# Kernel optimization log

Measured on AMD Instinct MI355X. Metric: run time of the kernel, lower is better.

## Reference

```python
import jax, jax.numpy as jnp
import numpy as np

N_ITER = 5
B = 16            # graphs
NPG = 3125        # nodes per graph
EPG = 50000       # edges per graph
N_NODES = B * NPG # 50000
E = B * EPG       # 800000
F = 32            # f_e = f_x = f_u
H = 64            # hidden


def _lin(key, fan_in, fan_out):
    k1, k2 = jax.random.split(key)
    s = 1.0 / np.sqrt(fan_in)
    W = jax.random.uniform(k1, (fan_in, fan_out), jnp.float32, -s, s)
    b = jax.random.uniform(k2, (fan_out,), jnp.float32, -s, s)
    return W, b


def setup_inputs() -> dict:
    key = jax.random.key(0)
    ks = jax.random.split(key, 12)
    x = jax.random.normal(ks[0], (N_NODES, F), jnp.float32)
    edge_attr = jax.random.normal(ks[1], (E, F), jnp.float32)
    y = jax.random.normal(ks[2], (B, F), jnp.float32)
    # within-graph random edges: graph g owns nodes [g*NPG, (g+1)*NPG)
    off = (jnp.arange(B, dtype=jnp.int32) * NPG)[:, None]          # [B,1]
    src = jax.random.randint(ks[3], (B, EPG), 0, NPG, jnp.int32) + off
    dst = jax.random.randint(ks[4], (B, EPG), 0, NPG, jnp.int32) + off
    edge_index = jnp.stack([src.reshape(-1), dst.reshape(-1)])      # [2,E]
    batch = jnp.repeat(jnp.arange(B, dtype=jnp.int32), NPG)         # [N]
    # shared GN-block parameters (one block reused for all N_ITER steps)
    We1, be1 = _lin(ks[5], F + 2 * F + F, H)   # edge MLP: [src,dst,e,u[b]]
    We2, be2 = _lin(ks[6], H, F)
    Wn1, bn1 = _lin(ks[7], F + F + F, H)       # node MLP: [x,e_agg,u[b]]
    Wn2, bn2 = _lin(ks[8], H, F)
    Wg1, bg1 = _lin(ks[9], F + F + F, H)       # global MLP: [x_agg,e_agg,u]
    Wg2, bg2 = _lin(ks[10], H, F)
    return dict(x=x, edge_attr=edge_attr, y=y,
                We1=We1, be1=be1, We2=We2, be2=be2,
                Wn1=Wn1, bn1=bn1, Wn2=Wn2, bn2=bn2,
                Wg1=Wg1, bg1=bg1, Wg2=Wg2, bg2=bg2,
                edge_index=edge_index, batch=batch)


def _mlp(h_in, W1, b1, W2, b2):
    return jax.nn.relu(h_in @ W1 + b1) @ W2 + b2


def _segment_mean(vals, seg, num):
    s = jax.ops.segment_sum(vals, seg, num_segments=num)
    c = jax.ops.segment_sum(jnp.ones((vals.shape[0], 1), vals.dtype), seg,
                            num_segments=num)
    return s / jnp.maximum(c, 1.0)


def _gn_forward(x, edge_attr, y, params, edge_index, batch):
    (We1, be1, We2, be2, Wn1, bn1, Wn2, bn2, Wg1, bg1, Wg2, bg2) = params
    row, col = edge_index[0], edge_index[1]
    e_batch = batch[row]
    for _ in range(N_ITER):  # shared-weight unrolled GN block
        # EdgeModel: phi_e([src, dest, e, u[batch_e]])
        e_in = jnp.concatenate([x[row], x[col], edge_attr, y[e_batch]], axis=1)
        edge_attr = _mlp(e_in, We1, be1, We2, be2)
        # NodeModel: mean of incoming edges (scatter over col)
        e_agg_node = _segment_mean(edge_attr, col, N_NODES)
        n_in = jnp.concatenate([x, e_agg_node, y[batch]], axis=1)
        x = _mlp(n_in, Wn1, bn1, Wn2, bn2)
        # GlobalModel: per-graph means of edges and nodes
        e_agg = _segment_mean(edge_attr, e_batch, B)
        x_agg = _segment_mean(x, batch, B)
        g_in = jnp.concatenate([x_agg, e_agg, y], axis=1)
        y = _mlp(g_in, Wg1, bg1, Wg2, bg2)
    return x, edge_attr, y


def reference(x, edge_attr, y,
              We1, be1, We2, be2,
              Wn1, bn1, Wn2, bn2,
              Wg1, bg1, Wg2, bg2,
              edge_index, batch):
    params = (We1, be1, We2, be2, Wn1, bn1, Wn2, bn2, Wg1, bg1, Wg2, bg2)
    return _gn_forward(x, edge_attr, y, params, edge_index, batch)
```

## Files before the change

### kernel.cpp

```cpp
#include <hip/hip_runtime.h>

#define NITER   5
#define B_G     16
#define NPG     3125
#define EPG     50000
#define NNODES  50000
#define NEDGES  800000
#define FD      32
#define HD      64

#define EDGE_TPG   391
#define EDGE_BLOCKS 1024

#define NODE_TPG   25
#define NODE_BLOCKS (B_G * NODE_TPG)

typedef __attribute__((ext_vector_type(4))) float f32x4;
typedef __attribute__((ext_vector_type(8))) short bf16x8;
typedef __attribute__((ext_vector_type(4))) unsigned int u32x4;

union FragU { bf16x8 v; unsigned int u[4]; u32x4 q; };

__device__ __forceinline__ void fsplit2(float a, float b,
                                        unsigned int& hi, unsigned int& lo) {
    unsigned int ua = __float_as_uint(a), ub = __float_as_uint(b);
    float la = a - __uint_as_float(ua & 0xffff0000u);
    float lb = b - __uint_as_float(ub & 0xffff0000u);
    hi = __builtin_amdgcn_perm(ub, ua, 0x07060302u);
    lo = __builtin_amdgcn_perm(__float_as_uint(lb), __float_as_uint(la), 0x07060302u);
}
__device__ __forceinline__ unsigned int fpack_hl(float v) {
    unsigned int uv = __float_as_uint(v);
    float lv = v - __uint_as_float(uv & 0xffff0000u);
    return __builtin_amdgcn_perm(__float_as_uint(lv), uv, 0x07060302u);
}
__device__ __forceinline__ bf16x8 ldfrag(const unsigned int* p) {
    FragU t; t.q = *(const u32x4*)p; return t.v;
}

__global__ __launch_bounds__(1024) void wsplit_kernel(
    const float* __restrict__ We1, const float* __restrict__ We2,
    const float* __restrict__ Wn1, const float* __restrict__ Wn2,
    unsigned int* __restrict__ wsp)
{
    for (int item = threadIdx.x; item < 1792; item += 1024) {
        const float* W; unsigned int* dst; int lda, s, n, l;
        if (item < 768)       { int f = item >> 6;          l = item & 63; s = f >> 2; n = f & 3; W = We1; lda = 64; dst = wsp + f * 512; }
        else if (item < 1024) { int f = (item - 768) >> 6;  l = item & 63; s = f >> 1; n = f & 1; W = We2; lda = 32; dst = wsp + 6144 + f * 512; }
        else if (item < 1536) { int f = (item - 1024) >> 6; l = item & 63; s = f >> 2; n = f & 3; W = Wn1; lda = 64; dst = wsp + 8192 + f * 512; }
        else                  { int f = (item - 1536) >> 6; l = item & 63; s = f >> 1; n = f & 1; W = Wn2; lda = 32; dst = wsp + 12288 + f * 512; }
        int lm = l & 15, lg = l >> 4;
        int rowbase = s * 32 + lg * 8;
        int col = n * 16 + lm;
        #pragma unroll
        for (int p = 0; p < 4; ++p) {
            float a = W[(rowbase + 2 * p) * lda + col];
            float b = W[(rowbase + 2 * p + 1) * lda + col];
            unsigned int hi, lo;
            fsplit2(a, b, hi, lo);
            dst[l * 4 + p] = hi;
            dst[256 + l * 4 + p] = lo;
        }
    }
}

__global__ __launch_bounds__(256) void xsplit_kernel(
    const float* __restrict__ xin, unsigned int* __restrict__ x_sp)
{
    int t = blockIdx.x * 256 + threadIdx.x;
    if (t >= NNODES * 4) return;
    int n = t >> 2, c = t & 3;
    long base = (long)n * 32 + c * 8;
    f32x4 a = *(const f32x4*)(xin + base);
    f32x4 b = *(const f32x4*)(xin + base + 4);
    unsigned int h[4], lo[4];
    fsplit2(a[0], a[1], h[0], lo[0]);
    fsplit2(a[2], a[3], h[1], lo[1]);
    fsplit2(b[0], b[1], h[2], lo[2]);
    fsplit2(b[2], b[3], h[3], lo[3]);
    *(u32x4*)(x_sp + (long)n * 32 + c * 4)      = (u32x4){h[0], h[1], h[2], h[3]};
    *(u32x4*)(x_sp + (long)n * 32 + 16 + c * 4) = (u32x4){lo[0], lo[1], lo[2], lo[3]};
}


__global__ __launch_bounds__(256) void count_kernel(const int* __restrict__ coli,
                                                    int* __restrict__ cnt)
{
    int e = blockIdx.x * 256 + threadIdx.x;
    if (e < NEDGES) atomicAdd(&cnt[coli[e]], 1);
}

__global__ __launch_bounds__(1024) void scan_blocks_kernel(const int* __restrict__ deg,
                                                           int* __restrict__ off,
                                                           int* __restrict__ bsum, int n)
{
    __shared__ int buf[1024];
    int tid = threadIdx.x;
    int idx = blockIdx.x * 1024 + tid;
    int v = (idx < n) ? deg[idx] : 0;
    buf[tid] = v;
    __syncthreads();
    for (int o = 1; o < 1024; o <<= 1) {
        int t = (tid >= o) ? buf[tid - o] : 0;
        __syncthreads();
        buf[tid] += t;
        __syncthreads();
    }
    if (idx < n) off[idx] = buf[tid] - v;
    if (tid == 1023) bsum[blockIdx.x] = buf[1023];
}

__global__ __launch_bounds__(64) void scan_carry_kernel(int* __restrict__ bsum,
                                                        int* __restrict__ off,
                                                        int nb, int n)
{
    if (threadIdx.x == 0) {
        int c = 0;
        for (int i = 0; i < nb; ++i) { int t = bsum[i]; bsum[i] = c; c += t; }
        off[n] = c;
    }
}

__global__ __launch_bounds__(1024) void scan_add_kernel(const int* __restrict__ bsum,
                                                        int* __restrict__ off, int n)
{
    int idx = blockIdx.x * 1024 + threadIdx.x;
    if (idx < n) off[idx] += bsum[blockIdx.x];
}

__global__ __launch_bounds__(256) void fill_kernel(const int* __restrict__ coli,
                                                   const int* __restrict__ off,
                                                   int* __restrict__ cursor,
                                                   int* __restrict__ csr)
{
    int e = blockIdx.x * 256 + threadIdx.x;
    if (e < NEDGES) {
        int c = coli[e];
        int pos = atomicAdd(&cursor[c], 1);
        csr[off[c] + pos] = e;
    }
}


__global__ __launch_bounds__(1024) void prep_kernel(
    const float* __restrict__ y,
    const float* __restrict__ We1, const float* __restrict__ be1,
    const float* __restrict__ Wn1, const float* __restrict__ bn1,
    float* __restrict__ cu_e, float* __restrict__ cu_n,
    float* __restrict__ xagg, float* __restrict__ eagg)
{
    int tid = threadIdx.x;
    if (tid < B_G * FD) xagg[tid] = 0.0f;
    else                eagg[tid - B_G * FD] = 0.0f;

    int g = tid >> 6;
    int j = tid & 63;
    float ae = be1[j];
    float an = bn1[j];
    for (int k = 0; k < FD; ++k) {
        float yv = y[g * FD + k];
        ae = fmaf(yv, We1[(96 + k) * HD + j], ae);
        an = fmaf(yv, Wn1[(64 + k) * HD + j], an);
    }
    cu_e[g * HD + j] = ae;
    cu_n[g * HD + j] = an;
}

__global__ __launch_bounds__(256) void edge_mfma_kernel(
    const unsigned int* __restrict__ x_sp,
    const float* __restrict__ ea_in,
    const int* __restrict__ rowi,
    const int* __restrict__ coli,
    const unsigned int* __restrict__ wsp,
    const float* __restrict__ be2,
    const float* __restrict__ cu_e,
    float* __restrict__ ea_out,
    float* __restrict__ eagg)
{
    __shared__ unsigned int h_lds[4][32][68];

    const int tid = threadIdx.x;
    const int wid = tid >> 6;
    const int l   = tid & 63;
    const int lm  = l & 15;
    const int lg  = l >> 4;
    const int koff = lg * 8;

    bf16x8 w1h[3][4], w1l[3][4];
    #pragma unroll
    for (int s = 0; s < 3; ++s)
        #pragma unroll
        for (int n = 0; n < 4; ++n) {
            const unsigned int* p = wsp + (s * 4 + n) * 512 + l * 4;
            w1h[s][n] = ldfrag(p);
            w1l[s][n] = ldfrag(p + 256);
        }
    bf16x8 w2h[2][2], w2l[2][2];
    #pragma unroll
    for (int s = 0; s < 2; ++s)
        #pragma unroll
        for (int n = 0; n < 2; ++n) {
            const unsigned int* p = wsp + 6144 + (s * 2 + n) * 512 + l * 4;
            w2h[s][n] = ldfrag(p);
            w2l[s][n] = ldfrag(p + 256);
        }
    float bias2[2];
    bias2[0] = be2[lm];
    bias2[1] = be2[16 + lm];

    const int b   = blockIdx.x;
    const int xcd = b & 7;
    const int i   = b >> 3;
    const int g   = 2 * xcd + (i >> 6);
    const int j0  = i & 63;
    const long gbase = (long)g * EPG;
    const long gend  = gbase + EPG;

    float bcu[4];
    #pragma unroll
    for (int n = 0; n < 4; ++n) bcu[n] = cu_e[g * HD + n * 16 + lm];

    auto idx_load = [&](int (&rr)[2], int (&cc)[2], int lt) {
        #pragma unroll
        for (int t = 0; t < 2; ++t) {
            long e = gbase + (long)lt * 128 + wid * 32 + t * 16 + lm;
            if (e >= gend) e = gend - 1;
            rr[t] = rowi[e];
            cc[t] = coli[e];
        }
    };
    auto x_load = [&](u32x4 (&xh)[2][2], u32x4 (&xl)[2][2],
                      const int (&rr)[2], const int (&cc)[2]) {
        #pragma unroll
        for (int t = 0; t < 2; ++t) {
            const unsigned int* pr = x_sp + (long)rr[t] * 32;
            const unsigned int* pc = x_sp + (long)cc[t] * 32;
            xh[t][0] = *(const u32x4*)(pr + lg * 4);
            xl[t][0] = *(const u32x4*)(pr + 16 + lg * 4);
            xh[t][1] = *(const u32x4*)(pc + lg * 4);
            xl[t][1] = *(const u32x4*)(pc + 16 + lg * 4);
        }
    };

    auto compute = [&](int lt, u32x4 (&xh)[2][2], u32x4 (&xl)[2][2]) {
        const long e0 = gbase + (long)lt * 128 + wid * 32;

        f32x4 vea[2][2];
        #pragma unroll
        for (int t = 0; t < 2; ++t) {
            long e = e0 + t * 16 + lm;
            if (e >= gend) e = gend - 1;
            const float* p2 = ea_in + e * FD + koff;
            vea[t][0] = *(const f32x4*)p2;
            vea[t][1] = *(const f32x4*)(p2 + 4);
        }

        f32x4 acc1[2][4];
        #pragma unroll
        for (int n = 0; n < 4; ++n)
            #pragma unroll
            for (int t = 0; t < 2; ++t)
                acc1[t][n] = (f32x4){bcu[n], bcu[n], bcu[n], bcu[n]};

        #pragma unroll
        for (int t = 0; t < 2; ++t)
            #pragma unroll
            for (int s = 0; s < 2; ++s) {
                FragU ah, al;
                ah.q = xh[t][s];
                al.q = xl[t][s];
                #pragma unroll
                for (int n = 0; n < 4; ++n) {
                    acc1[t][n] = __builtin_amdgcn_mfma_f32_16x16x32_bf16(ah.v, w1h[s][n], acc1[t][n], 0, 0, 0);
                    acc1[t][n] = __builtin_amdgcn_mfma_f32_16x16x32_bf16(ah.v, w1l[s][n], acc1[t][n], 0, 0, 0);
                    acc1[t][n] = __builtin_amdgcn_mfma_f32_16x16x32_bf16(al.v, w1h[s][n], acc1[t][n], 0, 0, 0);
                }
            }
        #pragma unroll
        for (int t = 0; t < 2; ++t) {
            FragU ah, al;
            #pragma unroll
            for (int q = 0; q < 2; ++q)
                #pragma unroll
                for (int p = 0; p < 2; ++p)
                    fsplit2(vea[t][q][2 * p], vea[t][q][2 * p + 1],
                            ah.u[q * 2 + p], al.u[q * 2 + p]);
            #pragma unroll
            for (int n = 0; n < 4; ++n) {
                acc1[t][n] = __builtin_amdgcn_mfma_f32_16x16x32_bf16(ah.v, w1h[2][n], acc1[t][n], 0, 0, 0);
                acc1[t][n] = __builtin_amdgcn_mfma_f32_16x16x32_bf16(ah.v, w1l[2][n], acc1[t][n], 0, 0, 0);
                acc1[t][n] = __builtin_amdgcn_mfma_f32_16x16x32_bf16(al.v, w1h[2][n], acc1[t][n], 0, 0, 0);
            }
        }

        #pragma unroll
        for (int t = 0; t < 2; ++t)
            #pragma unroll
            for (int n = 0; n < 4; ++n)
                #pragma unroll
                for (int r = 0; r < 4; ++r)
                    h_lds[wid][t * 16 + lg * 4 + r][n * 16 + lm] =
                        fpack_hl(fmaxf(acc1[t][n][r], 0.0f));
        asm volatile("s_waitcnt lgkmcnt(0)" ::: "memory");
        __builtin_amdgcn_sched_barrier(0);

        f32x4 acc2[2][2];
        #pragma unroll
        for (int n = 0; n < 2; ++n)
            #pragma unroll
            for (int t = 0; t < 2; ++t)
                acc2[t][n] = (f32x4){bias2[n], bias2[n], bias2[n], bias2[n]};
        #pragma unroll
        for (int t = 0; t < 2; ++t)
            #pragma unroll
            for (int s = 0; s < 2; ++s) {
                const unsigned int* hp = &h_lds[wid][t * 16 + lm][s * 32 + koff];
                unsigned int u0 = hp[0], u1 = hp[1], u2 = hp[2], u3 = hp[3];
                unsigned int u4 = hp[4], u5 = hp[5], u6 = hp[6], u7 = hp[7];
                FragU ah, al;
                ah.u[0] = __builtin_amdgcn_perm(u1, u0, 0x05040100u);
                ah.u[1] = __builtin_amdgcn_perm(u3, u2, 0x05040100u);
                ah.u[2] = __builtin_amdgcn_perm(u5, u4, 0x05040100u);
                ah.u[3] = __builtin_amdgcn_perm(u7, u6, 0x05040100u);
                al.u[0] = __builtin_amdgcn_perm(u1, u0, 0x07060302u);
                al.u[1] = __builtin_amdgcn_perm(u3, u2, 0x07060302u);
                al.u[2] = __builtin_amdgcn_perm(u5, u4, 0x07060302u);
                al.u[3] = __builtin_amdgcn_perm(u7, u6, 0x07060302u);
                #pragma unroll
                for (int n = 0; n < 2; ++n) {
                    acc2[t][n] = __builtin_amdgcn_mfma_f32_16x16x32_bf16(ah.v, w2h[s][n], acc2[t][n], 0, 0, 0);
                    acc2[t][n] = __builtin_amdgcn_mfma_f32_16x16x32_bf16(ah.v, w2l[s][n], acc2[t][n], 0, 0, 0);
                    acc2[t][n] = __builtin_amdgcn_mfma_f32_16x16x32_bf16(al.v, w2h[s][n], acc2[t][n], 0, 0, 0);
                }
            }

        #pragma unroll
        for (int t = 0; t < 2; ++t)
            #pragma unroll
            for (int r = 0; r < 4; ++r) {
                long e = e0 + t * 16 + lg * 4 + r;
                if (e < gend) {
                    ea_out[e * FD + lm]      = acc2[t][0][r];
                    ea_out[e * FD + 16 + lm] = acc2[t][1][r];
                }
            }

        #pragma unroll
        for (int n = 0; n < 2; ++n) {
            float s = 0.0f;
            #pragma unroll
            for (int t = 0; t < 2; ++t)
                #pragma unroll
                for (int r = 0; r < 4; ++r) {
                    long e = e0 + t * 16 + lg * 4 + r;
                    s += (e < gend) ? acc2[t][n][r] : 0.0f;
                }
            s += __shfl_xor(s, 16, 64);
            s += __shfl_xor(s, 32, 64);
            if (lg == 0) atomicAdd(&eagg[g * FD + n * 16 + lm], s);
        }
    };

    int rrA[2], ccA[2], rrB[2], ccB[2];
    u32x4 xhA[2][2], xlA[2][2], xhB[2][2], xlB[2][2];

    idx_load(rrA, ccA, j0);
    x_load(xhA, xlA, rrA, ccA);
    idx_load(rrB, ccB, j0 + 64);

    auto step = [&](int lt,
                    u32x4 (&xh)[2][2], u32x4 (&xl)[2][2], int (&rrD)[2], int (&ccD)[2],
                    u32x4 (&xhN)[2][2], u32x4 (&xlN)[2][2], int (&rrN)[2], int (&ccN)[2]) {
        idx_load(rrD, ccD, lt + 128);
        x_load(xhN, xlN, rrN, ccN);
        compute(lt, xh, xl);
    };

    for (int lt = j0; lt < EDGE_TPG; lt += 128) {
        step(lt, xhA, xlA, rrA, ccA, xhB, xlB, rrB, ccB);
        if (lt + 64 < EDGE_TPG)
            step(lt + 64, xhB, xlB, rrB, ccB, xhA, xlA, rrA, ccA);
    }
}

__global__ __launch_bounds__(256) void agg_kernel(
    const float* __restrict__ ea,
    const int* __restrict__ off,
    const int* __restrict__ csr,
    float* __restrict__ e_mean)
{
    int wid = threadIdx.x >> 6;
    int l   = threadIdx.x & 63;
    int rq  = l >> 3;
    int q   = l & 7;
    int n = blockIdx.x * 4 + wid;
    int s0 = off[n], s1 = off[n + 1];
    int deg = s1 - s0;

    f32x4 acc = {0.0f, 0.0f, 0.0f, 0.0f};
    if (deg > 0) {
        int cl = (l < deg) ? l : 0;
        int cidx = csr[s0 + cl];
        #pragma unroll
        for (int r = 0; r < 8; ++r) {
            int src = r * 8 + rq;
            int eid = __shfl(cidx, src, 64);
            if (src < deg) {
                f32x4 v = *(const f32x4*)(ea + (long)eid * FD + q * 4);
                acc += v;
            }
        }
        if (deg > 64) {
            for (int i = s0 + 64; i < s1; i += 8) {
                int ii = i + rq;
                if (ii < s1) {
                    int eid = csr[ii];
                    acc += *(const f32x4*)(ea + (long)eid * FD + q * 4);
                }
            }
        }
    }
    #pragma unroll
    for (int m = 8; m < 64; m <<= 1) {
        acc[0] += __shfl_xor(acc[0], m, 64);
        acc[1] += __shfl_xor(acc[1], m, 64);
        acc[2] += __shfl_xor(acc[2], m, 64);
        acc[3] += __shfl_xor(acc[3], m, 64);
    }
    float inv = 1.0f / (float)(deg > 1 ? deg : 1);
    if (l < 8) {
        f32x4 o = {acc[0] * inv, acc[1] * inv, acc[2] * inv, acc[3] * inv};
        *(f32x4*)(e_mean + (long)n * FD + q * 4) = o;
    }
}

__global__ __launch_bounds__(256) void node_mfma_kernel(
    const float* __restrict__ x_in,
    const float* __restrict__ e_mean,
    const unsigned int* __restrict__ wsp,
    const float* __restrict__ bn2,
    const float* __restrict__ cu_n,
    float* __restrict__ x_out,
    float* __restrict__ xagg)
{
    __shared__ unsigned int h_lds[4][32][68];

    const int tid = threadIdx.x;
    const int wid = tid >> 6;
    const int l   = tid & 63;
    const int lm  = l & 15;
    const int lg  = l >> 4;
    const int koff = lg * 8;

    bf16x8 w1h[2][4], w1l[2][4];
    #pragma unroll
    for (int s = 0; s < 2; ++s)
        #pragma unroll
        for (int n = 0; n < 4; ++n) {
            const unsigned int* p = wsp + (s * 4 + n) * 512 + l * 4;
            w1h[s][n] = ldfrag(p);
            w1l[s][n] = ldfrag(p + 256);
        }
    bf16x8 w2h[2][2], w2l[2][2];
    #pragma unroll
    for (int s = 0; s < 2; ++s)
        #pragma unroll
        for (int n = 0; n < 2; ++n) {
            const unsigned int* p = wsp + 4096 + (s * 2 + n) * 512 + l * 4;
            w2h[s][n] = ldfrag(p);
            w2l[s][n] = ldfrag(p + 256);
        }
    float bias2[2];
    bias2[0] = bn2[lm];
    bias2[1] = bn2[16 + lm];

    const int g  = blockIdx.x / NODE_TPG;
    const int lt = blockIdx.x - g * NODE_TPG;
    const int nb = lt * 128 + wid * 32;

    f32x4 va[2][2][2];
    #pragma unroll
    for (int t = 0; t < 2; ++t) {
        int rl = nb + t * 16 + lm;
        if (rl > NPG - 1) rl = NPG - 1;
        long node = (long)g * NPG + rl;
        const float* p0 = x_in   + node * FD + koff;
        const float* p1 = e_mean + node * FD + koff;
        va[t][0][0] = *(const f32x4*)p0; va[t][0][1] = *(const f32x4*)(p0 + 4);
        va[t][1][0] = *(const f32x4*)p1; va[t][1][1] = *(const f32x4*)(p1 + 4);
    }

    f32x4 acc1[2][4];
    #pragma unroll
    for (int n = 0; n < 4; ++n) {
        float b = cu_n[g * HD + n * 16 + lm];
        #pragma unroll
        for (int t = 0; t < 2; ++t) acc1[t][n] = (f32x4){b, b, b, b};
    }

    #pragma unroll
    for (int t = 0; t < 2; ++t) {
        #pragma unroll
        for (int s = 0; s < 2; ++s) {
            FragU ah, al;
            #pragma unroll
            for (int q = 0; q < 2; ++q)
                #pragma unroll
                for (int p = 0; p < 2; ++p)
                    fsplit2(va[t][s][q][2 * p], va[t][s][q][2 * p + 1],
                            ah.u[q * 2 + p], al.u[q * 2 + p]);
            #pragma unroll
            for (int n = 0; n < 4; ++n) {
                acc1[t][n] = __builtin_amdgcn_mfma_f32_16x16x32_bf16(ah.v, w1h[s][n], acc1[t][n], 0, 0, 0);
                acc1[t][n] = __builtin_amdgcn_mfma_f32_16x16x32_bf16(ah.v, w1l[s][n], acc1[t][n], 0, 0, 0);
                acc1[t][n] = __builtin_amdgcn_mfma_f32_16x16x32_bf16(al.v, w1h[s][n], acc1[t][n], 0, 0, 0);
            }
        }
    }

    #pragma unroll
    for (int t = 0; t < 2; ++t)
        #pragma unroll
        for (int n = 0; n < 4; ++n)
            #pragma unroll
            for (int r = 0; r < 4; ++r)
                h_lds[wid][t * 16 + lg * 4 + r][n * 16 + lm] =
                    fpack_hl(fmaxf(acc1[t][n][r], 0.0f));
    asm volatile("s_waitcnt lgkmcnt(0)" ::: "memory");
    __builtin_amdgcn_sched_barrier(0);

    f32x4 acc2[2][2];
    #pragma unroll
    for (int n = 0; n < 2; ++n) {
        #pragma unroll
        for (int t = 0; t < 2; ++t) acc2[t][n] = (f32x4){bias2[n], bias2[n], bias2[n], bias2[n]};
    }
    #pragma unroll
    for (int t = 0; t < 2; ++t) {
        #pragma unroll
        for (int s = 0; s < 2; ++s) {
            const unsigned int* hp = &h_lds[wid][t * 16 + lm][s * 32 + koff];
            unsigned int u0 = hp[0], u1 = hp[1], u2 = hp[2], u3 = hp[3];
            unsigned int u4 = hp[4], u5 = hp[5], u6 = hp[6], u7 = hp[7];
            FragU ah, al;
            ah.u[0] = __builtin_amdgcn_perm(u1, u0, 0x05040100u);
            ah.u[1] = __builtin_amdgcn_perm(u3, u2, 0x05040100u);
            ah.u[2] = __builtin_amdgcn_perm(u5, u4, 0x05040100u);
            ah.u[3] = __builtin_amdgcn_perm(u7, u6, 0x05040100u);
            al.u[0] = __builtin_amdgcn_perm(u1, u0, 0x07060302u);
            al.u[1] = __builtin_amdgcn_perm(u3, u2, 0x07060302u);
            al.u[2] = __builtin_amdgcn_perm(u5, u4, 0x07060302u);
            al.u[3] = __builtin_amdgcn_perm(u7, u6, 0x07060302u);
            #pragma unroll
            for (int n = 0; n < 2; ++n) {
                acc2[t][n] = __builtin_amdgcn_mfma_f32_16x16x32_bf16(ah.v, w2h[s][n], acc2[t][n], 0, 0, 0);
                acc2[t][n] = __builtin_amdgcn_mfma_f32_16x16x32_bf16(ah.v, w2l[s][n], acc2[t][n], 0, 0, 0);
                acc2[t][n] = __builtin_amdgcn_mfma_f32_16x16x32_bf16(al.v, w2h[s][n], acc2[t][n], 0, 0, 0);
            }
        }
    }

    #pragma unroll
    for (int t = 0; t < 2; ++t)
        #pragma unroll
        for (int r = 0; r < 4; ++r) {
            int rl = nb + t * 16 + lg * 4 + r;
            if (rl < NPG) {
                long node = (long)g * NPG + rl;
                x_out[node * FD + lm]      = acc2[t][0][r];
                x_out[node * FD + 16 + lm] = acc2[t][1][r];
            }
        }

    #pragma unroll
    for (int n = 0; n < 2; ++n) {
        float s = 0.0f;
        #pragma unroll
        for (int t = 0; t < 2; ++t)
            #pragma unroll
            for (int r = 0; r < 4; ++r) {
                int rl = nb + t * 16 + lg * 4 + r;
                s += (rl < NPG) ? acc2[t][n][r] : 0.0f;
            }
        s += __shfl_xor(s, 16, 64);
        s += __shfl_xor(s, 32, 64);
        if (lg == 0) atomicAdd(&xagg[g * FD + n * 16 + lm], s);
    }
}

__global__ __launch_bounds__(1024) void global_kernel(
    const float* __restrict__ y_in,
    float* __restrict__ xagg, float* __restrict__ eagg,
    const float* __restrict__ Wg1, const float* __restrict__ bg1,
    const float* __restrict__ Wg2, const float* __restrict__ bg2,
    const float* __restrict__ We1, const float* __restrict__ be1,
    const float* __restrict__ Wn1, const float* __restrict__ bn1,
    float* __restrict__ y_out,
    float* __restrict__ cu_e, float* __restrict__ cu_n)
{
    __shared__ float in_lds[B_G][100];
    __shared__ float h_lds2[B_G][HD + 1];
    __shared__ float y_lds[B_G][FD];
    int tid = threadIdx.x;
    for (int idx = tid; idx < B_G * 96; idx += 1024) {
        int g2 = idx / 96, k = idx % 96;
        float v;
        if (k < 32)      v = xagg[g2 * 32 + k] * (1.0f / NPG);
        else if (k < 64) v = eagg[g2 * 32 + (k - 32)] * (1.0f / EPG);
        else             v = y_in[g2 * 32 + (k - 64)];
        in_lds[g2][k] = v;
    }
    __syncthreads();
    int g = tid >> 6, j = tid & 63;
    float h = bg1[j];
    for (int k = 0; k < 96; ++k)
        h = fmaf(in_lds[g][k], Wg1[k * HD + j], h);
    h_lds2[g][j] = fmaxf(h, 0.0f);
    __syncthreads();
    if (j < FD) {
        float o = bg2[j];
        for (int k = 0; k < HD; ++k)
            o = fmaf(h_lds2[g][k], Wg2[k * FD + j], o);
        y_out[g * FD + j] = o;
        y_lds[g][j] = o;
    }
    __syncthreads();
    float ae = be1[j];
    float an = bn1[j];
    for (int k = 0; k < FD; ++k) {
        float yv = y_lds[g][k];
        ae = fmaf(yv, We1[(96 + k) * HD + j], ae);
        an = fmaf(yv, Wn1[(64 + k) * HD + j], an);
    }
    cu_e[g * HD + j] = ae;
    cu_n[g * HD + j] = an;
    if (tid < B_G * FD)            xagg[tid] = 0.0f;
    else if (tid < 2 * B_G * FD)   eagg[tid - B_G * FD] = 0.0f;
}


extern "C" void kernel_launch(void* const* d_in, const int* in_sizes, int n_in,
                              void* d_out, int out_size, void* d_ws, size_t ws_size,
                              hipStream_t stream)
{
    const float* x0  = (const float*)d_in[0];
    const float* ea0 = (const float*)d_in[1];
    const float* y0  = (const float*)d_in[2];
    const float* We1 = (const float*)d_in[3];
    const float* be1 = (const float*)d_in[4];
    const float* We2 = (const float*)d_in[5];
    const float* be2 = (const float*)d_in[6];
    const float* Wn1 = (const float*)d_in[7];
    const float* bn1 = (const float*)d_in[8];
    const float* Wn2 = (const float*)d_in[9];
    const float* bn2 = (const float*)d_in[10];
    const float* Wg1 = (const float*)d_in[11];
    const float* bg1 = (const float*)d_in[12];
    const float* Wg2 = (const float*)d_in[13];
    const float* bg2 = (const float*)d_in[14];
    const int*   ei  = (const int*)d_in[15];
    const int* rowi = ei;
    const int* coli = ei + NEDGES;

    float* out_x  = (float*)d_out;
    float* out_ea = out_x + (size_t)NNODES * FD;
    float* out_y  = out_ea + (size_t)NEDGES * FD;

    char* ws = (char*)d_ws;
    int*   off    = (int*)(ws + 0);
    int*   cursor = (int*)(ws + 200192);
    int*   csr    = (int*)(ws + 400384);
    float* xagg   = (float*)(ws + 3600384);
    float* eagg   = xagg + B_G * FD;
    float* cu_e   = (float*)(ws + 3604480);
    float* cu_n   = cu_e + B_G * HD;
    float* e_mean = (float*)(ws + 3612672);
    unsigned int* wsp = (unsigned int*)(ws + 10012672);
    int*   bsum   = (int*)(ws + 10070016);
    unsigned int* x_sp = (unsigned int*)(ws + 10070272);

    wsplit_kernel<<<1, 1024, 0, stream>>>(We1, We2, Wn1, Wn2, wsp);
    hipMemsetAsync(cursor, 0, NNODES * sizeof(int), stream);
    count_kernel<<<(NEDGES + 255) / 256, 256, 0, stream>>>(coli, cursor);
    scan_blocks_kernel<<<49, 1024, 0, stream>>>(cursor, off, bsum, NNODES);
    scan_carry_kernel<<<1, 64, 0, stream>>>(bsum, off, 49, NNODES);
    scan_add_kernel<<<49, 1024, 0, stream>>>(bsum, off, NNODES);
    hipMemsetAsync(cursor, 0, NNODES * sizeof(int), stream);
    fill_kernel<<<(NEDGES + 255) / 256, 256, 0, stream>>>(coli, off, cursor, csr);

    prep_kernel<<<1, 1024, 0, stream>>>(y0, We1, be1, Wn1, bn1,
                                        cu_e, cu_n, xagg, eagg);

    for (int it = 0; it < NITER; ++it) {
        const float* xc  = (it == 0) ? x0  : out_x;
        const float* eac = (it == 0) ? ea0 : out_ea;
        const float* yc  = (it == 0) ? y0  : out_y;

        xsplit_kernel<<<(NNODES * 4 + 255) / 256, 256, 0, stream>>>(xc, x_sp);
        edge_mfma_kernel<<<EDGE_BLOCKS, 256, 0, stream>>>(x_sp, eac, rowi, coli,
                                                          wsp, be2, cu_e,
                                                          out_ea, eagg);
        agg_kernel<<<NNODES / 4, 256, 0, stream>>>(out_ea, off, csr, e_mean);
        node_mfma_kernel<<<NODE_BLOCKS, 256, 0, stream>>>(xc, e_mean,
                                                          wsp + 8192, bn2, cu_n,
                                                          out_x, xagg);
        global_kernel<<<1, 1024, 0, stream>>>(yc, xagg, eagg,
                                              Wg1, bg1, Wg2, bg2,
                                              We1, be1, Wn1, bn1,
                                              out_y, cu_e, cu_n);
    }
}
```

Baseline: 667.2 us.

## Transpose edge MLP MFMA to keep hidden in registers, weights in LDS

The edge kernel now computes the transposed product (weights as the A operand, edge features as B), so the first-layer output fragment maps directly onto the second layer's B operand. This removes the LDS round-trip for the hidden activations. Weight fragments move from registers into a shared-memory copy loaded once per block, and the We2 split layout is reordered to match. Per-edge outputs become vectorized f32x4 stores, and the per-graph edge sum is accumulated across tiles with a single atomic reduction at the end. The trade-off is extra LDS reads of weights inside the loop and a simpler one-tile index prefetch in place of the double-buffered x prefetch.

Result: slower. 711.3 us (+6.6%).

```diff
diff --git a/kernel.cpp b/kernel.cpp
--- a/kernel.cpp
+++ b/kernel.cpp
@@ -37,6 +37,9 @@
 __device__ __forceinline__ bf16x8 ldfrag(const unsigned int* p) {
     FragU t; t.q = *(const u32x4*)p; return t.v;
 }
+__device__ __forceinline__ f32x4 mfma16(bf16x8 a, bf16x8 b, f32x4 c) {
+    return __builtin_amdgcn_mfma_f32_16x16x32_bf16(a, b, c, 0, 0, 0);
+}
 
 __global__ __launch_bounds__(1024) void wsplit_kernel(
     const float* __restrict__ We1, const float* __restrict__ We2,
@@ -44,22 +47,56 @@
     unsigned int* __restrict__ wsp)
 {
     for (int item = threadIdx.x; item < 1792; item += 1024) {
-        const float* W; unsigned int* dst; int lda, s, n, l;
-        if (item < 768)       { int f = item >> 6;          l = item & 63; s = f >> 2; n = f & 3; W = We1; lda = 64; dst = wsp + f * 512; }
-        else if (item < 1024) { int f = (item - 768) >> 6;  l = item & 63; s = f >> 1; n = f & 1; W = We2; lda = 32; dst = wsp + 6144 + f * 512; }
-        else if (item < 1536) { int f = (item - 1024) >> 6; l = item & 63; s = f >> 2; n = f & 3; W = Wn1; lda = 64; dst = wsp + 8192 + f * 512; }
-        else                  { int f = (item - 1536) >> 6; l = item & 63; s = f >> 1; n = f & 1; W = Wn2; lda = 32; dst = wsp + 12288 + f * 512; }
+        int l = item & 63;
         int lm = l & 15, lg = l >> 4;
-        int rowbase = s * 32 + lg * 8;
-        int col = n * 16 + lm;
-        #pragma unroll
-        for (int p = 0; p < 4; ++p) {
-            float a = W[(rowbase + 2 * p) * lda + col];
-            float b = W[(rowbase + 2 * p + 1) * lda + col];
-            unsigned int hi, lo;
-            fsplit2(a, b, hi, lo);
-            dst[l * 4 + p] = hi;
-            dst[256 + l * 4 + p] = lo;
+        if (item < 768) {
+            int f = item >> 6; int s = f >> 2, n = f & 3;
+            unsigned int* dst = wsp + f * 512;
+            int rowbase = s * 32 + lg * 8;
+            int col = n * 16 + lm;
+            #pragma unroll
+            for (int p = 0; p < 4; ++p) {
+                unsigned int hi, lo;
+                fsplit2(We1[(rowbase + 2*p) * HD + col],
+                        We1[(rowbase + 2*p + 1) * HD + col], hi, lo);
+                dst[l*4 + p] = hi; dst[256 + l*4 + p] = lo;
+            }
+        } else if (item < 1024) {
+            int f = (item - 768) >> 6; int s2 = f >> 1, n2 = f & 1;
+            unsigned int* dst = wsp + 6144 + f * 512;
+            int col = n2 * 16 + lm;
+            #pragma unroll
+            for (int p = 0; p < 4; ++p) {
+                int m  = 2 * s2 + (p >> 1);
+                int j0 = m * 16 + lg * 4 + ((2*p) & 3);
+                unsigned int hi, lo;
+                fsplit2(We2[j0 * FD + col], We2[(j0 + 1) * FD + col], hi, lo);
+                dst[l*4 + p] = hi; dst[256 + l*4 + p] = lo;
+            }
+        } else if (item < 1536) {
+            int f = (item - 1024) >> 6; int s = f >> 2, n = f & 3;
+            unsigned int* dst = wsp + 8192 + f * 512;
+            int rowbase = s * 32 + lg * 8;
+            int col = n * 16 + lm;
+            #pragma unroll
+            for (int p = 0; p < 4; ++p) {
+                unsigned int hi, lo;
+                fsplit2(Wn1[(rowbase + 2*p) * HD + col],
+                        Wn1[(rowbase + 2*p + 1) * HD + col], hi, lo);
+                dst[l*4 + p] = hi; dst[256 + l*4 + p] = lo;
+            }
+        } else {
+            int f = (item - 1536) >> 6; int s = f >> 1, n = f & 1;
+            unsigned int* dst = wsp + 12288 + f * 512;
+            int rowbase = s * 32 + lg * 8;
+            int col = n * 16 + lm;
+            #pragma unroll
+            for (int p = 0; p < 4; ++p) {
+                unsigned int hi, lo;
+                fsplit2(Wn2[(rowbase + 2*p) * FD + col],
+                        Wn2[(rowbase + 2*p + 1) * FD + col], hi, lo);
+                dst[l*4 + p] = hi; dst[256 + l*4 + p] = lo;
+            }
         }
     }
 }
@@ -177,36 +214,21 @@
     float* __restrict__ ea_out,
     float* __restrict__ eagg)
 {
-    __shared__ unsigned int h_lds[4][32][68];
+    __shared__ __align__(16) unsigned int wlds[8192];
+    {
+        const u32x4* src = (const u32x4*)wsp;
+        u32x4* dst = (u32x4*)wlds;
+        #pragma unroll
+        for (int i = 0; i < 8; ++i)
+            dst[threadIdx.x + i * 256] = src[threadIdx.x + i * 256];
+    }
+    __syncthreads();
 
     const int tid = threadIdx.x;
     const int wid = tid >> 6;
     const int l   = tid & 63;
     const int lm  = l & 15;
     const int lg  = l >> 4;
-    const int koff = lg * 8;
-
-    bf16x8 w1h[3][4], w1l[3][4];
-    #pragma unroll
-    for (int s = 0; s < 3; ++s)
-        #pragma unroll
-        for (int n = 0; n < 4; ++n) {
-            const unsigned int* p = wsp + (s * 4 + n) * 512 + l * 4;
-            w1h[s][n] = ldfrag(p);
-            w1l[s][n] = ldfrag(p + 256);
-        }
-    bf16x8 w2h[2][2], w2l[2][2];
-    #pragma unroll
-    for (int s = 0; s < 2; ++s)
-        #pragma unroll
-        for (int n = 0; n < 2; ++n) {
-            const unsigned int* p = wsp + 6144 + (s * 2 + n) * 512 + l * 4;
-            w2h[s][n] = ldfrag(p);
-            w2l[s][n] = ldfrag(p + 256);
-        }
-    float bias2[2];
-    bias2[0] = be2[lm];
-    bias2[1] = be2[16 + lm];
 
     const int b   = blockIdx.x;
     const int xcd = b & 7;
@@ -216,171 +238,154 @@
     const long gbase = (long)g * EPG;
     const long gend  = gbase + EPG;
 
-    float bcu[4];
-    #pragma unroll
-    for (int n = 0; n < 4; ++n) bcu[n] = cu_e[g * HD + n * 16 + lm];
-
-    auto idx_load = [&](int (&rr)[2], int (&cc)[2], int lt) {
-        #pragma unroll
-        for (int t = 0; t < 2; ++t) {
-            long e = gbase + (long)lt * 128 + wid * 32 + t * 16 + lm;
-            if (e >= gend) e = gend - 1;
-            rr[t] = rowi[e];
-            cc[t] = coli[e];
-        }
-    };
-    auto x_load = [&](u32x4 (&xh)[2][2], u32x4 (&xl)[2][2],
-                      const int (&rr)[2], const int (&cc)[2]) {
+    f32x4 bias1[4];
+    #pragma unroll
+    for (int m = 0; m < 4; ++m)
+        bias1[m] = *(const f32x4*)(cu_e + g * HD + m * 16 + lg * 4);
+    f32x4 bias2[2];
+    #pragma unroll
+    for (int n2 = 0; n2 < 2; ++n2)
+        bias2[n2] = *(const f32x4*)(be2 + n2 * 16 + lg * 4);
+
+    f32x4 eacc[2] = {{0,0,0,0},{0,0,0,0}};
+
+    int nrr[2], ncc[2];
+    #pragma unroll
+    for (int t = 0; t < 2; ++t) {
+        long e = gbase + (long)j0 * 128 + wid * 32 + t * 16 + lm;
+        if (e >= gend) e = gend - 1;
+        nrr[t] = rowi[e]; ncc[t] = coli[e];
+    }
+
+    for (int lt = j0; lt < EDGE_TPG; lt += 64) {
+        int rr[2] = {nrr[0], nrr[1]}, cc[2] = {ncc[0], ncc[1]};
+        int nlt = lt + 64;
+        if (nlt < EDGE_TPG) {
+            #pragma unroll
+            for (int t = 0; t < 2; ++t) {
+                long e = gbase + (long)nlt * 128 + wid * 32 + t * 16 + lm;
+                if (e >= gend) e = gend - 1;
+                nrr[t] = rowi[e]; ncc[t] = coli[e];
+            }
+        }
+        const long e0 = gbase + (long)lt * 128 + wid * 32;
+
+        u32x4 bxh[2][2], bxl[2][2];
         #pragma unroll
         for (int t = 0; t < 2; ++t) {
             const unsigned int* pr = x_sp + (long)rr[t] * 32;
             const unsigned int* pc = x_sp + (long)cc[t] * 32;
-            xh[t][0] = *(const u32x4*)(pr + lg * 4);
-            xl[t][0] = *(const u32x4*)(pr + 16 + lg * 4);
-            xh[t][1] = *(const u32x4*)(pc + lg * 4);
-            xl[t][1] = *(const u32x4*)(pc + 16 + lg * 4);
-        }
-    };
-
-    auto compute = [&](int lt, u32x4 (&xh)[2][2], u32x4 (&xl)[2][2]) {
-        const long e0 = gbase + (long)lt * 128 + wid * 32;
-
+            bxh[t][0] = *(const u32x4*)(pr + lg * 4);
+            bxl[t][0] = *(const u32x4*)(pr + 16 + lg * 4);
+            bxh[t][1] = *(const u32x4*)(pc + lg * 4);
+            bxl[t][1] = *(const u32x4*)(pc + 16 + lg * 4);
+        }
         f32x4 vea[2][2];
         #pragma unroll
         for (int t = 0; t < 2; ++t) {
             long e = e0 + t * 16 + lm;
             if (e >= gend) e = gend - 1;
-            const float* p2 = ea_in + e * FD + koff;
-            vea[t][0] = *(const f32x4*)p2;
-            vea[t][1] = *(const f32x4*)(p2 + 4);
+            const float* p = ea_in + e * FD + lg * 8;
+            vea[t][0] = *(const f32x4*)p;
+            vea[t][1] = *(const f32x4*)(p + 4);
         }
 
         f32x4 acc1[2][4];
         #pragma unroll
-        for (int n = 0; n < 4; ++n)
-            #pragma unroll
-            for (int t = 0; t < 2; ++t)
-                acc1[t][n] = (f32x4){bcu[n], bcu[n], bcu[n], bcu[n]};
-
+        for (int m = 0; m < 4; ++m) { acc1[0][m] = bias1[m]; acc1[1][m] = bias1[m]; }
+
+        #pragma unroll
+        for (int s = 0; s < 2; ++s)
+            #pragma unroll
+            for (int m = 0; m < 4; ++m) {
+                bf16x8 wh = ldfrag(wlds + (s * 4 + m) * 512 + l * 4);
+                bf16x8 wl = ldfrag(wlds + (s * 4 + m) * 512 + 256 + l * 4);
+                #pragma unroll
+                for (int t = 0; t < 2; ++t) {
+                    FragU bh, bl; bh.q = bxh[t][s]; bl.q = bxl[t][s];
+                    acc1[t][m] = mfma16(wh, bh.v, acc1[t][m]);
+                    acc1[t][m] = mfma16(wl, bh.v, acc1[t][m]);
+                    acc1[t][m] = mfma16(wh, bl.v, acc1[t][m]);
+                }
+            }
+        FragU beh[2], bel[2];
         #pragma unroll
         for (int t = 0; t < 2; ++t)
-            #pragma unroll
-            for (int s = 0; s < 2; ++s) {
-                FragU ah, al;
-                ah.q = xh[t][s];
-                al.q = xl[t][s];
-                #pragma unroll
-                for (int n = 0; n < 4; ++n) {
-                    acc1[t][n] = __builtin_amdgcn_mfma_f32_16x16x32_bf16(ah.v, w1h[s][n], acc1[t][n], 0, 0, 0);
-                    acc1[t][n] = __builtin_amdgcn_mfma_f32_16x16x32_bf16(ah.v, w1l[s][n], acc1[t][n], 0, 0, 0);
-                    acc1[t][n] = __builtin_amdgcn_mfma_f32_16x16x32_bf16(al.v, w1h[s][n], acc1[t][n], 0, 0, 0);
-                }
-            }
-        #pragma unroll
-        for (int t = 0; t < 2; ++t) {
-            FragU ah, al;
             #pragma unroll
             for (int q = 0; q < 2; ++q)
                 #pragma unroll
                 for (int p = 0; p < 2; ++p)
                     fsplit2(vea[t][q][2 * p], vea[t][q][2 * p + 1],
-                            ah.u[q * 2 + p], al.u[q * 2 + p]);
-            #pragma unroll
-            for (int n = 0; n < 4; ++n) {
-                acc1[t][n] = __builtin_amdgcn_mfma_f32_16x16x32_bf16(ah.v, w1h[2][n], acc1[t][n], 0, 0, 0);
-                acc1[t][n] = __builtin_amdgcn_mfma_f32_16x16x32_bf16(ah.v, w1l[2][n], acc1[t][n], 0, 0, 0);
-                acc1[t][n] = __builtin_amdgcn_mfma_f32_16x16x32_bf16(al.v, w1h[2][n], acc1[t][n], 0, 0, 0);
-            }
-        }
-
+                            beh[t].u[q * 2 + p], bel[t].u[q * 2 + p]);
+        #pragma unroll
+        for (int m = 0; m < 4; ++m) {
+            bf16x8 wh = ldfrag(wlds + (8 + m) * 512 + l * 4);
+            bf16x8 wl = ldfrag(wlds + (8 + m) * 512 + 256 + l * 4);
+            #pragma unroll
+            for (int t = 0; t < 2; ++t) {
+                acc1[t][m] = mfma16(wh, beh[t].v, acc1[t][m]);
+                acc1[t][m] = mfma16(wl, beh[t].v, acc1[t][m]);
+                acc1[t][m] = mfma16(wh, bel[t].v, acc1[t][m]);
+            }
+        }
+
+        FragU b2h[2][2], b2l[2][2];
         #pragma unroll
         for (int t = 0; t < 2; ++t)
             #pragma unroll
-            for (int n = 0; n < 4; ++n)
+            for (int s2 = 0; s2 < 2; ++s2)
                 #pragma unroll
-                for (int r = 0; r < 4; ++r)
-                    h_lds[wid][t * 16 + lg * 4 + r][n * 16 + lm] =
-                        fpack_hl(fmaxf(acc1[t][n][r], 0.0f));
-        asm volatile("s_waitcnt lgkmcnt(0)" ::: "memory");
-        __builtin_amdgcn_sched_barrier(0);
+                for (int p = 0; p < 4; ++p) {
+                    int m = 2 * s2 + (p >> 1);
+                    int r = (2 * p) & 3;
+                    float a = fmaxf(acc1[t][m][r], 0.0f);
+                    float c = fmaxf(acc1[t][m][r + 1], 0.0f);
+                    fsplit2(a, c, b2h[t][s2].u[p], b2l[t][s2].u[p]);
+                }
 
         f32x4 acc2[2][2];
         #pragma unroll
-        for (int n = 0; n < 2; ++n)
-            #pragma unroll
-            for (int t = 0; t < 2; ++t)
-                acc2[t][n] = (f32x4){bias2[n], bias2[n], bias2[n], bias2[n]};
-        #pragma unroll
-        for (int t = 0; t < 2; ++t)
-            #pragma unroll
-            for (int s = 0; s < 2; ++s) {
-                const unsigned int* hp = &h_lds[wid][t * 16 + lm][s * 32 + koff];
-                unsigned int u0 = hp[0], u1 = hp[1], u2 = hp[2], u3 = hp[3];
-                unsigned int u4 = hp[4], u5 = hp[5], u6 = hp[6], u7 = hp[7];
-                FragU ah, al;
-                ah.u[0] = __builtin_amdgcn_perm(u1, u0, 0x05040100u);
-                ah.u[1] = __builtin_amdgcn_perm(u3, u2, 0x05040100u);
-                ah.u[2] = __builtin_amdgcn_perm(u5, u4, 0x05040100u);
-                ah.u[3] = __builtin_amdgcn_perm(u7, u6, 0x05040100u);
-                al.u[0] = __builtin_amdgcn_perm(u1, u0, 0x07060302u);
-                al.u[1] = __builtin_amdgcn_perm(u3, u2, 0x07060302u);
-                al.u[2] = __builtin_amdgcn_perm(u5, u4, 0x07060302u);
-                al.u[3] = __builtin_amdgcn_perm(u7, u6, 0x07060302u);
+        for (int n2 = 0; n2 < 2; ++n2) { acc2[0][n2] = bias2[n2]; acc2[1][n2] = bias2[n2]; }
+        #pragma unroll
+        for (int s2 = 0; s2 < 2; ++s2)
+            #pragma unroll
+            for (int n2 = 0; n2 < 2; ++n2) {
+                bf16x8 wh = ldfrag(wlds + 6144 + (s2 * 2 + n2) * 512 + l * 4);
+                bf16x8 wl = ldfrag(wlds + 6144 + (s2 * 2 + n2) * 512 + 256 + l * 4);
                 #pragma unroll
-                for (int n = 0; n < 2; ++n) {
-                    acc2[t][n] = __builtin_amdgcn_mfma_f32_16x16x32_bf16(ah.v, w2h[s][n], acc2[t][n], 0, 0, 0);
-                    acc2[t][n] = __builtin_amdgcn_mfma_f32_16x16x32_bf16(ah.v, w2l[s][n], acc2[t][n], 0, 0, 0);
-                    acc2[t][n] = __builtin_amdgcn_mfma_f32_16x16x32_bf16(al.v, w2h[s][n], acc2[t][n], 0, 0, 0);
+                for (int t = 0; t < 2; ++t) {
+                    acc2[t][n2] = mfma16(wh, b2h[t][s2].v, acc2[t][n2]);
+                    acc2[t][n2] = mfma16(wl, b2h[t][s2].v, acc2[t][n2]);
+                    acc2[t][n2] = mfma16(wh, b2l[t][s2].v, acc2[t][n2]);
                 }
             }
 
-        #pragma unroll
-        for (int t = 0; t < 2; ++t)
-            #pragma unroll
-            for (int r = 0; r < 4; ++r) {
-                long e = e0 + t * 16 + lg * 4 + r;
-                if (e < gend) {
-                    ea_out[e * FD + lm]      = acc2[t][0][r];
-                    ea_out[e * FD + 16 + lm] = acc2[t][1][r];
-                }
-            }
-
-        #pragma unroll
-        for (int n = 0; n < 2; ++n) {
-            float s = 0.0f;
-            #pragma unroll
-            for (int t = 0; t < 2; ++t)
-                #pragma unroll
-                for (int r = 0; r < 4; ++r) {
-                    long e = e0 + t * 16 + lg * 4 + r;
-                    s += (e < gend) ? acc2[t][n][r] : 0.0f;
-                }
-            s += __shfl_xor(s, 16, 64);
-            s += __shfl_xor(s, 32, 64);
-            if (lg == 0) atomicAdd(&eagg[g * FD + n * 16 + lm], s);
-        }
-    };
-
-    int rrA[2], ccA[2], rrB[2], ccB[2];
-    u32x4 xhA[2][2], xlA[2][2], xhB[2][2], xlB[2][2];
-
-    idx_load(rrA, ccA, j0);
-    x_load(xhA, xlA, rrA, ccA);
-    idx_load(rrB, ccB, j0 + 64);
-
-    auto step = [&](int lt,
-                    u32x4 (&xh)[2][2], u32x4 (&xl)[2][2], int (&rrD)[2], int (&ccD)[2],
-                    u32x4 (&xhN)[2][2], u32x4 (&xlN)[2][2], int (&rrN)[2], int (&ccN)[2]) {
-        idx_load(rrD, ccD, lt + 128);
-        x_load(xhN, xlN, rrN, ccN);
-        compute(lt, xh, xl);
-    };
-
-    for (int lt = j0; lt < EDGE_TPG; lt += 128) {
-        step(lt, xhA, xlA, rrA, ccA, xhB, xlB, rrB, ccB);
-        if (lt + 64 < EDGE_TPG)
-            step(lt + 64, xhB, xlB, rrB, ccB, xhA, xlA, rrA, ccA);
-    }
+        int cnt = (int)(gend - e0);
+        #pragma unroll
+        for (int t = 0; t < 2; ++t) {
+            int local = t * 16 + lm;
+            bool v = local < cnt;
+            if (v) {
+                float* po = ea_out + (e0 + local) * FD + lg * 4;
+                *(f32x4*)po        = acc2[t][0];
+                *(f32x4*)(po + 16) = acc2[t][1];
+                eacc[0] += acc2[t][0];
+                eacc[1] += acc2[t][1];
+            }
+        }
+    }
+
+    #pragma unroll
+    for (int n2 = 0; n2 < 2; ++n2)
+        #pragma unroll
+        for (int r = 0; r < 4; ++r) {
+            float vv = eacc[n2][r];
+            vv += __shfl_xor(vv, 1, 64);
+            vv += __shfl_xor(vv, 2, 64);
+            vv += __shfl_xor(vv, 4, 64);
+            vv += __shfl_xor(vv, 8, 64);
+            if (lm == 0) atomicAdd(&eagg[g * FD + n2 * 16 + lg * 4 + r], vv);
+        }
 }
 
 __global__ __launch_bounds__(256) void agg_kernel(
@@ -511,9 +516,9 @@
                             ah.u[q * 2 + p], al.u[q * 2 + p]);
             #pragma unroll
             for (int n = 0; n < 4; ++n) {
-                acc1[t][n] = __builtin_amdgcn_mfma_f32_16x16x32_bf16(ah.v, w1h[s][n], acc1[t][n], 0, 0, 0);
-                acc1[t][n] = __builtin_amdgcn_mfma_f32_16x16x32_bf16(ah.v, w1l[s][n], acc1[t][n], 0, 0, 0);
-                acc1[t][n] = __builtin_amdgcn_mfma_f32_16x16x32_bf16(al.v, w1h[s][n], acc1[t][n], 0, 0, 0);
+                acc1[t][n] = mfma16(ah.v, w1h[s][n], acc1[t][n]);
+                acc1[t][n] = mfma16(ah.v, w1l[s][n], acc1[t][n]);
+                acc1[t][n] = mfma16(al.v, w1h[s][n], acc1[t][n]);
             }
         }
     }
@@ -553,9 +558,9 @@
             al.u[3] = __builtin_amdgcn_perm(u7, u6, 0x07060302u);
             #pragma unroll
             for (int n = 0; n < 2; ++n) {
-                acc2[t][n] = __builtin_amdgcn_mfma_f32_16x16x32_bf16(ah.v, w2h[s][n], acc2[t][n], 0, 0, 0);
-                acc2[t][n] = __builtin_amdgcn_mfma_f32_16x16x32_bf16(ah.v, w2l[s][n], acc2[t][n], 0, 0, 0);
-                acc2[t][n] = __builtin_amdgcn_mfma_f32_16x16x32_bf16(al.v, w2h[s][n], acc2[t][n], 0, 0, 0);
+                acc2[t][n] = mfma16(ah.v, w2h[s][n], acc2[t][n]);
+                acc2[t][n] = mfma16(ah.v, w2l[s][n], acc2[t][n]);
+                acc2[t][n] = mfma16(al.v, w2h[s][n], acc2[t][n]);
             }
         }
     }
```
